# Kernel optimization log

Hardware: AMD Instinct MI355X
Metric: run time of the kernel (lower is better)

Reference implementation:

```python
import jax, jax.numpy as jnp
import numpy as np

B, T, D, H = 8, 1024, 768, 12
HD = D // H          # 64 head dim
WINDOW = 768         # sliding-window width hardcoded in the block
EPS = 1e-5

def _layer_norm(x, w, b):
    mu = jnp.mean(x, axis=-1, keepdims=True)
    var = jnp.mean(jnp.square(x - mu), axis=-1, keepdims=True)
    return (x - mu) * jax.lax.rsqrt(var + EPS) * w + b

def setup_inputs() -> dict:
    key = jax.random.key(0)
    ks = jax.random.split(key, 16)
    s = 0.02
    return {
        "x": jax.random.normal(ks[0], (B, T, D), jnp.float32),
        "attn_mask": jnp.ones((B, T), jnp.int32),
        "ln1_w": jnp.ones((D,), jnp.float32),
        "ln1_b": jnp.zeros((D,), jnp.float32),
        "w_attn": jax.random.normal(ks[1], (D, 3 * D), jnp.float32) * s,
        "b_attn": jnp.zeros((3 * D,), jnp.float32),
        "w_proj": jax.random.normal(ks[2], (D, D), jnp.float32) * s,
        "b_proj": jnp.zeros((D,), jnp.float32),
        "ln2_w": jnp.ones((D,), jnp.float32),
        "ln2_b": jnp.zeros((D,), jnp.float32),
        "w_fc": jax.random.normal(ks[3], (D, 4 * D), jnp.float32) * s,
        "b_fc": jnp.zeros((4 * D,), jnp.float32),
        "w_fc_proj": jax.random.normal(ks[4], (4 * D, D), jnp.float32) * s,
        "b_fc_proj": jnp.zeros((D,), jnp.float32),
    }

def reference(x, attn_mask, ln1_w, ln1_b, w_attn, b_attn, w_proj, b_proj,
              ln2_w, ln2_b, w_fc, b_fc, w_fc_proj, b_fc_proj):
    dtype = x.dtype
    # --- attention sub-block ---
    x1 = _layer_norm(x, ln1_w, ln1_b)
    qkv = x1 @ w_attn + b_attn                       # [B,T,3D]
    q, k, v = jnp.split(qkv, 3, axis=-1)
    q = q.reshape(B, T, H, HD).transpose(0, 2, 1, 3)  # [B,H,T,HD]
    k = k.reshape(B, T, H, HD).transpose(0, 2, 1, 3)
    v = v.reshape(B, T, H, HD).transpose(0, 2, 1, 3)
    # causal + sliding-window + padding mask (additive bias, as in source)
    i = jnp.arange(T)[:, None]
    j = jnp.arange(T)[None, :]
    keep = (j <= i) & (j >= i - WINDOW + 1)           # [T,T]
    keep = keep[None, None] & (attn_mask.astype(bool))[:, None, None, :]  # [B,1,T,T]
    mask_bias = jnp.where(keep, jnp.zeros((), dtype), jnp.full((), jnp.finfo(dtype).min, dtype))
    scale = 1.0 / np.sqrt(HD)
    scores = jnp.einsum('bhqd,bhkd->bhqk', q, k) * scale + mask_bias
    probs = jax.nn.softmax(scores, axis=-1)
    attn = jnp.einsum('bhqk,bhkd->bhqd', probs, v)    # [B,H,T,HD]
    attn = attn.transpose(0, 2, 1, 3).reshape(B, T, D)
    a = attn @ w_proj + b_proj
    x = x + a
    # --- MLP sub-block ---
    x3 = _layer_norm(x, ln2_w, ln2_b)
    h = jax.nn.gelu(x3 @ w_fc + b_fc, approximate=False)
    m = h @ w_fc_proj + b_fc_proj
    return x + m
```

## Files before the change

kernel.cpp:

```cpp
#include <hip/hip_runtime.h>
#include <hip/hip_bf16.h>
#include <math.h>

#define NB 8
#define NT 1024
#define ND 768
#define NH 12
#define HD 64
#define WINDOW 768
#define LN_EPS 1e-5f
#define NEGF -3.4028234663852886e38f
#define SCL2 0.18033688011112042f

static const int BT = NB * NT;

typedef __bf16 bf16x8 __attribute__((ext_vector_type(8)));
typedef float  f32x4  __attribute__((ext_vector_type(4)));
typedef unsigned short ushort_t;

__device__ __forceinline__ unsigned short f2bf(float f) {
    __hip_bfloat16 h = __float2bfloat16(f);
    return __builtin_bit_cast(unsigned short, h);
}

__device__ __forceinline__ void load_lds16(const void* g, void* l) {
    __builtin_amdgcn_global_load_lds((const __attribute__((address_space(1))) unsigned int*)g,
                                     (__attribute__((address_space(3))) unsigned int*)l,
                                     16, 0, 0);
}

__device__ __forceinline__ bf16x8 ds_read16(const ushort_t* p) {
    bf16x8 r;
    unsigned a = (unsigned)(size_t)(const __attribute__((address_space(3))) ushort_t*)p;
    asm volatile("ds_read_b128 %0, %1" : "=v"(r) : "v"(a));
    return r;
}

__global__ __launch_bounds__(256) void transpose_all(const float* __restrict__ w0, ushort_t* __restrict__ t0v,
                                                     const float* __restrict__ w1, ushort_t* __restrict__ t1v,
                                                     const float* __restrict__ w2, ushort_t* __restrict__ t2v,
                                                     const float* __restrict__ w3, ushort_t* __restrict__ t3v) {
    int bid = blockIdx.x;
    const float* w; ushort_t* wt; int K, N;
    if (bid < 1728)                    { w = w0; wt = t0v; K = 768;  N = 2304; }
    else if ((bid -= 1728) < 576)      { w = w1; wt = t1v; K = 768;  N = 768;  }
    else if ((bid -= 576) < 2304)      { w = w2; wt = t2v; K = 768;  N = 3072; }
    else       { bid -= 2304;            w = w3; wt = t3v; K = 3072; N = 768;  }
    const int nxt = N / 32;
    const int n0 = (bid % nxt) * 32, k0 = (bid / nxt) * 32;
    __shared__ float t[32][33];
    const int tx = threadIdx.x & 31, ty = threadIdx.x >> 5;
    for (int r = ty; r < 32; r += 8)
        t[r][tx] = w[(size_t)(k0 + r) * N + n0 + tx];
    __syncthreads();
    for (int r = ty; r < 32; r += 8)
        wt[(size_t)(n0 + r) * K + k0 + tx] = f2bf(t[tx][r]);
}

__global__ __launch_bounds__(256) void transpose_v(const ushort_t* __restrict__ qkvb,
                                                   ushort_t* __restrict__ vT) {
    const int t0 = blockIdx.x * 64;
    const int h = blockIdx.y, b = blockIdx.z;
    __shared__ ushort_t sm[64 * 72];
    const int tid = threadIdx.x;
    #pragma unroll
    for (int p = 0; p < 2; p++) {
        int idx = p * 256 + tid;
        int r = idx >> 3, c = idx & 7;
        *(bf16x8*)&sm[r * 72 + c * 8] =
            *(const bf16x8*)(qkvb + (size_t)(b * NT + t0 + r) * (3 * ND) + 2 * ND + h * HD + c * 8);
    }
    __syncthreads();
    #pragma unroll
    for (int p = 0; p < 2; p++) {
        int idx = p * 256 + tid;
        int d = idx >> 3, c2 = idx & 7;
        ushort_t tmp[8];
        #pragma unroll
        for (int j = 0; j < 8; j++) {
            int kp = c2 * 8 + j;
            int key = ((kp & 1) << 4) | ((kp >> 1) & 15) | (kp & 32);
            tmp[j] = sm[key * 72 + d];
        }
        *(bf16x8*)(vT + ((size_t)((b * NH + h) * HD + d)) * NT + t0 + c2 * 8) = *(bf16x8*)tmp;
    }
}

__global__ __launch_bounds__(256) void ln_kernel(const float* __restrict__ x,
                                                 const float* __restrict__ w,
                                                 const float* __restrict__ b,
                                                 ushort_t* __restrict__ out) {
    const int row  = blockIdx.x * 4 + (threadIdx.x >> 6);
    const int lane = threadIdx.x & 63;
    const float* xr = x + (size_t)row * ND;

    float4 v[3];
    #pragma unroll
    for (int s = 0; s < 3; s++) v[s] = *(const float4*)(xr + s * 256 + lane * 4);

    float sum = 0.f;
    #pragma unroll
    for (int s = 0; s < 3; s++) sum += v[s].x + v[s].y + v[s].z + v[s].w;
    #pragma unroll
    for (int off = 1; off < 64; off <<= 1) sum += __shfl_xor(sum, off, 64);
    const float mu = sum * (1.0f / ND);

    float var = 0.f;
    #pragma unroll
    for (int s = 0; s < 3; s++) {
        float a0 = v[s].x - mu, a1 = v[s].y - mu, a2 = v[s].z - mu, a3 = v[s].w - mu;
        var += a0 * a0 + a1 * a1 + a2 * a2 + a3 * a3;
    }
    #pragma unroll
    for (int off = 1; off < 64; off <<= 1) var += __shfl_xor(var, off, 64);
    const float rstd = rsqrtf(var * (1.0f / ND) + LN_EPS);

    #pragma unroll
    for (int s = 0; s < 3; s++) {
        const int col = s * 256 + lane * 4;
        float4 w4 = *(const float4*)(w + col);
        float4 b4 = *(const float4*)(b + col);
        ushort4 r;
        r.x = f2bf((v[s].x - mu) * rstd * w4.x + b4.x);
        r.y = f2bf((v[s].y - mu) * rstd * w4.y + b4.y);
        r.z = f2bf((v[s].z - mu) * rstd * w4.z + b4.z);
        r.w = f2bf((v[s].w - mu) * rstd * w4.w + b4.w);
        *(ushort4*)(out + (size_t)row * ND + col) = r;
    }
}

template <int EPI>
__global__ __launch_bounds__(256) void gemm_bt(const ushort_t* __restrict__ A,
                                               const ushort_t* __restrict__ Bt,
                                               const float* __restrict__ bias,
                                               const float* __restrict__ resid,
                                               void* __restrict__ Cout,
                                               int M, int N, int K) {
    __shared__ __align__(16) ushort_t smem[2][2][128 * 32];

    const int tid  = threadIdx.x;
    const int bm   = blockIdx.y * 128;
    const int bn   = blockIdx.x * 128;
    const int lane = tid & 63;
    const int wave = tid >> 6;
    const int wm   = (wave & 1) * 64;
    const int wn   = (wave >> 1) * 64;
    const int fcol = lane & 15;
    const int quad = lane >> 4;

    f32x4 acc[4][4] = {};

    const int srow = tid >> 2, scg = (tid & 3) * 8;

    auto issue = [&](int k0, int buf) {
        #pragma unroll
        for (int p = 0; p < 2; p++) {
            const int row = srow + p * 64;
            const int flat = (p * 256 + tid) * 8;
            load_lds16(A  + (size_t)(bm + row) * K + k0 + scg, &smem[buf][0][flat]);
            load_lds16(Bt + (size_t)(bn + row) * K + k0 + scg, &smem[buf][1][flat]);
        }
    };

    issue(0, 0);
    const int KT = K >> 5;
    for (int kt = 0; kt < KT; kt++) {
        const int cur = kt & 1;
        __syncthreads();
        if (kt + 1 < KT) issue((kt + 1) << 5, cur ^ 1);

        bf16x8 a[4], b[4];
        #pragma unroll
        for (int i = 0; i < 4; i++)
            a[i] = *(const bf16x8*)&smem[cur][0][(wm + i * 16 + fcol) * 32 + quad * 8];
        #pragma unroll
        for (int j = 0; j < 4; j++)
            b[j] = *(const bf16x8*)&smem[cur][1][(wn + j * 16 + fcol) * 32 + quad * 8];
        #pragma unroll
        for (int i = 0; i < 4; i++)
            #pragma unroll
            for (int j = 0; j < 4; j++)
                acc[i][j] = __builtin_amdgcn_mfma_f32_16x16x32_bf16(a[i], b[j], acc[i][j], 0, 0, 0);
    }

    if (EPI == 1) {
        #pragma unroll
        for (int j = 0; j < 4; j++) {
            const int gcol = bn + wn + j * 16 + fcol;
            const float bs = bias[gcol];
            #pragma unroll
            for (int i = 0; i < 4; i++) {
                #pragma unroll
                for (int r = 0; r < 4; r++) {
                    const int grow = bm + wm + i * 16 + quad * 4 + r;
                    float val = acc[i][j][r] + bs + resid[(size_t)grow * N + gcol];
                    ((float*)Cout)[(size_t)grow * N + gcol] = val;
                }
            }
        }
    } else {
        __syncthreads();
        ushort_t* Cs = &smem[0][0][0] + wave * (64 * 40);
        #pragma unroll
        for (int hh = 0; hh < 2; hh++) {
            #pragma unroll
            for (int jj = 0; jj < 2; jj++) {
                const int j = hh * 2 + jj;
                const float bs = bias[bn + wn + j * 16 + fcol];
                #pragma unroll
                for (int i = 0; i < 4; i++) {
                    #pragma unroll
                    for (int r = 0; r < 4; r++) {
                        float val = acc[i][j][r] + bs;
                        if (EPI == 2) {
                            float y = 0.7978845608028654f * (val + 0.044715f * val * val * val);
                            float t = 1.0f - 2.0f / (1.0f + __expf(2.0f * y));
                            val = 0.5f * val * (1.0f + t);
                        }
                        const int lr = i * 16 + quad * 4 + r;
                        Cs[lr * 40 + jj * 16 + fcol] = f2bf(val);
                    }
                }
            }
            #pragma unroll
            for (int p = 0; p < 4; p++) {
                const int cid = p * 64 + lane;
                const int lr = cid >> 2, ck = cid & 3;
                bf16x8 vv = *(const bf16x8*)&Cs[lr * 40 + ck * 8];
                *(bf16x8*)((ushort_t*)Cout + (size_t)(bm + wm + lr) * N + bn + wn + hh * 32 + ck * 8) = vv;
            }
        }
    }
}

template <int EPI, int NN, int KK>
__global__ __launch_bounds__(512, 2) void gemm256(const ushort_t* __restrict__ A,
                                                  const ushort_t* __restrict__ Bt,
                                                  const float* __restrict__ bias,
                                                  ushort_t* __restrict__ Cout) {
    extern __shared__ __align__(16) ushort_t lds[];

    const int tid  = threadIdx.x;
    const int lane = tid & 63;
    const int wave = tid >> 6;
    const int wr   = wave >> 2;
    const int wn   = wave & 3;
    const int fcol = lane & 15;
    const int quad = lane >> 4;

    const int nwg  = gridDim.x * gridDim.y;
    const int flat = blockIdx.y * gridDim.x + blockIdx.x;
    const int q8   = nwg >> 3;
    const int swz  = (flat & 7) * q8 + (flat >> 3);
    const int bm   = (swz / gridDim.x) * 256;
    const int bn   = (swz % gridDim.x) * 256;

    constexpr int KT  = KK >> 6;
    constexpr int NIT = KT >> 1;

    f32x4 acc[8][4] = {};
    bf16x8 ra[4][2];
    bf16x8 rb0[2][2], rb1[2][2];

    ushort_t* const Ab = lds;
    ushort_t* const Bb = lds + 32768;

    auto stA = [&](int kt, int h) {
        ushort_t* dst = Ab + ((((kt & 1) << 1) | h) << 13);
        const int kk = (kt < KT ? kt : 0) << 6;
        #pragma unroll
        for (int p = 0; p < 2; p++) {
            const int f = (p << 9) + tid;
            const int r = f >> 3, c = (f & 7) ^ (r & 7);
            const int gr = bm + ((r >> 6) << 7) + (h << 6) + (r & 63);
            load_lds16(A + (size_t)gr * KK + kk + c * 8, dst + f * 8);
        }
    };
    auto stB = [&](int kt, int h) {
        ushort_t* dst = Bb + ((((kt & 1) << 1) | h) << 13);
        const int kk = (kt < KT ? kt : 0) << 6;
        #pragma unroll
        for (int p = 0; p < 2; p++) {
            const int f = (p << 9) + tid;
            const int r = f >> 3, c = (f & 7) ^ (r & 7);
            const int gr = bn + ((r >> 5) << 6) + (h << 5) + (r & 31);
            load_lds16(Bt + (size_t)gr * KK + kk + c * 8, dst + f * 8);
        }
    };

#define SOFF(r, c) ((((r) << 3) + (((c) ^ ((r) & 7)))) << 3)
#define LOAD_A(PAR, MH) { const ushort_t* s_ = Ab + ((((PAR) << 1) | (MH)) << 13);   \
    _Pragma("unroll") for (int i2 = 0; i2 < 4; i2++)                                 \
    _Pragma("unroll") for (int ks = 0; ks < 2; ks++)                                 \
        ra[i2][ks] = ds_read16(&s_[SOFF(wr * 64 + i2 * 16 + fcol, ks * 4 + quad)]); }
#define LOAD_B(PAR, NH, RB) { const ushort_t* s_ = Bb + ((((PAR) << 1) | (NH)) << 13); \
    _Pragma("unroll") for (int j2 = 0; j2 < 2; j2++)                                 \
    _Pragma("unroll") for (int ks = 0; ks < 2; ks++)                                 \
        RB[j2][ks] = ds_read16(&s_[SOFF(wn * 32 + j2 * 16 + fcol, ks * 4 + quad)]); }
#define MMA(MH, NH, RB) {                                                            \
    __builtin_amdgcn_s_barrier();                                                    \
    asm volatile("s_waitcnt lgkmcnt(0)" ::: "memory");                               \
    __builtin_amdgcn_sched_barrier(0);                                               \
    __builtin_amdgcn_s_setprio(1);                                                   \
    _Pragma("unroll") for (int i2 = 0; i2 < 4; i2++)                                 \
    _Pragma("unroll") for (int j2 = 0; j2 < 2; j2++)                                 \
    _Pragma("unroll") for (int ks = 0; ks < 2; ks++)                                 \
        acc[(MH) * 4 + i2][(NH) * 2 + j2] = __builtin_amdgcn_mfma_f32_16x16x32_bf16( \
            ra[i2][ks], RB[j2][ks], acc[(MH) * 4 + i2][(NH) * 2 + j2], 0, 0, 0);     \
    __builtin_amdgcn_s_setprio(0);                                                   \
    __builtin_amdgcn_sched_barrier(0);                                               \
    __builtin_amdgcn_s_barrier(); }
#define VMW6() asm volatile("s_waitcnt vmcnt(6)" ::: "memory")

    stA(0, 0); stB(0, 0); stB(0, 1); stA(0, 1);
    stA(1, 0); stB(1, 0); stB(1, 1);
    VMW6();
    __builtin_amdgcn_s_barrier();

    #pragma unroll 1
    for (int it = 0; it < NIT; ++it) {
        const int E = it << 1, O = E + 1;
        LOAD_A(0, 0); LOAD_B(0, 0, rb0);
        stA(O, 1);
        MMA(0, 0, rb0);

        LOAD_B(0, 1, rb1);
        stA(E + 2, 0);
        MMA(0, 1, rb1);

        LOAD_A(0, 1);
        stB(E + 2, 0);
        MMA(1, 1, rb1);

        stB(E + 2, 1);
        VMW6();
        MMA(1, 0, rb0);

        LOAD_A(1, 0); LOAD_B(1, 0, rb0);
        stA(E + 2, 1);
        MMA(0, 0, rb0);

        LOAD_B(1, 1, rb1);
        stA(O + 2, 0);
        MMA(0, 1, rb1);

        LOAD_A(1, 1);
        stB(O + 2, 0);
        MMA(1, 1, rb1);

        stB(O + 2, 1);
        VMW6();
        MMA(1, 0, rb0);
    }

    asm volatile("s_waitcnt vmcnt(0)" ::: "memory");
    __builtin_amdgcn_s_barrier();

    ushort_t* Cs = lds + wave * (64 * 72);
    #pragma unroll
    for (int h = 0; h < 2; h++) {
        #pragma unroll
        for (int j = 0; j < 4; j++) {
            const float bs = bias[bn + wn * 64 + j * 16 + fcol];
            #pragma unroll
            for (int i2 = 0; i2 < 4; i2++) {
                #pragma unroll
                for (int r = 0; r < 4; r++) {
                    float val = acc[h * 4 + i2][j][r] + bs;
                    if (EPI == 2) {
                        float y = 0.7978845608028654f * (val + 0.044715f * val * val * val);
                        float t = 1.0f - 2.0f / (1.0f + __expf(2.0f * y));
                        val = 0.5f * val * (1.0f + t);
                    }
                    Cs[(i2 * 16 + quad * 4 + r) * 72 + j * 16 + fcol] = f2bf(val);
                }
            }
        }
        #pragma unroll
        for (int p = 0; p < 8; p++) {
            const int cid = (p << 6) + lane;
            const int lr = cid >> 3, ck = cid & 7;
            bf16x8 vv = *(const bf16x8*)&Cs[lr * 72 + ck * 8];
            *(bf16x8*)(Cout + (size_t)(bm + wr * 128 + h * 64 + lr) * NN + bn + wn * 64 + ck * 8) = vv;
        }
    }
#undef SOFF
#undef LOAD_A
#undef LOAD_B
#undef MMA
#undef VMW6
}

__global__ __launch_bounds__(256) void flash_attn_mfma(const ushort_t* __restrict__ qkvb,
                                                       const ushort_t* __restrict__ vT,
                                                       const int* __restrict__ amask,
                                                       ushort_t* __restrict__ out) {
    const int qt = 15 - blockIdx.x;
    const int h  = blockIdx.y;
    const int b  = blockIdx.z;
    const int q0 = qt * 64;

    __shared__ __align__(16) ushort_t QPs[64 * 64];
    __shared__ __align__(16) ushort_t Ks[2][64 * 64];
    __shared__ __align__(16) ushort_t Vts[2][64 * 64];

    const int tid  = threadIdx.x;
    const int lane = tid & 63;
    const int wave = tid >> 6;
    const int fcol = lane & 15;
    const int quad = lane >> 4;
    const int wq0  = wave * 16;

    #pragma unroll
    for (int p = 0; p < 2; p++) {
        int flat = p * 256 + tid;
        int r = flat >> 3, c = (flat & 7) ^ (r & 7);
        load_lds16(qkvb + (size_t)(b * NT + q0 + r) * (3 * ND) + h * HD + c * 8, &QPs[flat * 8]);
    }
    __syncthreads();

    bf16x8 aQ[2];
    {
        const int qr = wq0 + fcol;
        #pragma unroll
        for (int ks = 0; ks < 2; ks++) {
            int c = ks * 4 + quad;
            aQ[ks] = *(const bf16x8*)&QPs[qr * 64 + ((c ^ (qr & 7)) * 8)];
        }
    }

    bf16x8 bones;
    #pragma unroll
    for (int i = 0; i < 8; i++) bones[i] = (__bf16)1.0f;

    auto issueKV = [&](int cch, int buf) {
        const int kbase = cch * 64;
        #pragma unroll
        for (int p = 0; p < 2; p++) {
            int flat = p * 256 + tid;
            int r = flat >> 3, c = (flat & 7) ^ (r & 7);
            load_lds16(qkvb + (size_t)(b * NT + kbase + r) * (3 * ND) + ND + h * HD + c * 8,
                       &Ks[buf][flat * 8]);
            load_lds16(vT + ((size_t)((b * NH + h) * HD + r)) * NT + kbase + c * 8,
                       &Vts[buf][flat * 8]);
        }
    };

    f32x4 oacc[4] = {};
    f32x4 lacc = {};

    const int c_lo = (qt > 12) ? (qt - 12) : 0;
    issueKV(c_lo, 0);
    for (int cch = c_lo; cch <= qt; cch++) {
        const int cur = (cch - c_lo) & 1;
        const int kbase = cch * 64;
        __syncthreads();
        if (cch + 1 <= qt) issueKV(cch + 1, cur ^ 1);

        int am[4];
        #pragma unroll
        for (int jn = 0; jn < 4; jn++) am[jn] = amask[b * NT + kbase + jn * 16 + fcol];
        const int amok_lane = (am[0] != 0) & (am[1] != 0) & (am[2] != 0) & (am[3] != 0);
        const bool fast = (cch < qt) && (cch >= qt - 11) && __all(amok_lane);

        f32x4 sc[4] = {};
        #pragma unroll
        for (int ks = 0; ks < 2; ks++) {
            #pragma unroll
            for (int jn = 0; jn < 4; jn++) {
                const int kr = jn * 16 + fcol;
                bf16x8 bk = *(const bf16x8*)&Ks[cur][kr * 64 + (((ks * 4 + quad) ^ (kr & 7)) * 8)];
                sc[jn] = __builtin_amdgcn_mfma_f32_16x16x32_bf16(aQ[ks], bk, sc[jn], 0, 0, 0);
            }
        }

        float pvv[4][4];
        if (fast) {
            #pragma unroll
            for (int jn = 0; jn < 4; jn++)
                #pragma unroll
                for (int r = 0; r < 4; r++)
                    pvv[jn][r] = __builtin_amdgcn_exp2f(sc[jn][r] * SCL2);
        } else {
            #pragma unroll
            for (int jn = 0; jn < 4; jn++) {
                const int jg = kbase + jn * 16 + fcol;
                const bool amok = (am[jn] != 0);
                #pragma unroll
                for (int r = 0; r < 4; r++) {
                    const int ig = q0 + wq0 + quad * 4 + r;
                    bool keep = (jg <= ig) && (jg >= ig - (WINDOW - 1)) && amok;
                    float s = keep ? sc[jn][r] * SCL2 : -1e38f;
                    pvv[jn][r] = __builtin_amdgcn_exp2f(s);
                }
            }
        }

        #pragma unroll
        for (int half = 0; half < 2; half++) {
            const int cbase = half * 4 + (fcol >> 2);
            const int off = (fcol & 3) * 2;
            #pragma unroll
            for (int r = 0; r < 4; r++) {
                const int row = wq0 + quad * 4 + r;
                unsigned int pk = (unsigned int)f2bf(pvv[half * 2][r]) |
                                  ((unsigned int)f2bf(pvv[half * 2 + 1][r]) << 16);
                *(unsigned int*)&QPs[row * 64 + ((cbase ^ (row & 7)) * 8) + off] = pk;
            }
        }

        #pragma unroll
        for (int ks = 0; ks < 2; ks++) {
            const int pr = wq0 + fcol;
            bf16x8 ap = *(const bf16x8*)&QPs[pr * 64 + (((ks * 4 + quad) ^ (pr & 7)) * 8)];
            lacc = __builtin_amdgcn_mfma_f32_16x16x32_bf16(ap, bones, lacc, 0, 0, 0);
            #pragma unroll
            for (int jd = 0; jd < 4; jd++) {
                const int vr = jd * 16 + fcol;
                bf16x8 bv = *(const bf16x8*)&Vts[cur][vr * 64 + (((ks * 4 + quad) ^ (vr & 7)) * 8)];
                oacc[jd] = __builtin_amdgcn_mfma_f32_16x16x32_bf16(ap, bv, oacc[jd], 0, 0, 0);
            }
        }
    }

    #pragma unroll
    for (int r = 0; r < 4; r++) {
        const float inv = 1.0f / lacc[r];
        const size_t row = (size_t)(b * NT + q0 + wq0 + quad * 4 + r);
        #pragma unroll
        for (int jd = 0; jd < 4; jd++)
            out[row * ND + h * HD + jd * 16 + fcol] = f2bf(oacc[jd][r] * inv);
    }
}

extern "C" void kernel_launch(void* const* d_in, const int* in_sizes, int n_in,
                              void* d_out, int out_size, void* d_ws, size_t ws_size,
                              hipStream_t stream) {
    const float* x        = (const float*)d_in[0];
    const int*   amask    = (const int*)  d_in[1];
    const float* ln1_w    = (const float*)d_in[2];
    const float* ln1_b    = (const float*)d_in[3];
    const float* w_attn   = (const float*)d_in[4];
    const float* b_attn   = (const float*)d_in[5];
    const float* w_proj   = (const float*)d_in[6];
    const float* b_proj   = (const float*)d_in[7];
    const float* ln2_w    = (const float*)d_in[8];
    const float* ln2_b    = (const float*)d_in[9];
    const float* w_fc     = (const float*)d_in[10];
    const float* b_fc     = (const float*)d_in[11];
    const float* w_fcp    = (const float*)d_in[12];
    const float* b_fcp    = (const float*)d_in[13];
    float* out = (float*)d_out;

    ushort_t* ws = (ushort_t*)d_ws;
    ushort_t* qkvb   = ws;
    ushort_t* x1b    = qkvb + (size_t)BT * 3 * ND;
    ushort_t* attn_b = x1b + (size_t)BT * ND;
    ushort_t* hbuf   = attn_b + (size_t)BT * ND;
    ushort_t* vTb    = hbuf + (size_t)BT * 4 * ND;
    ushort_t* wA_T   = vTb + (size_t)BT * ND;
    ushort_t* wP_T   = wA_T + (size_t)2304 * 768;
    ushort_t* wF_T   = wP_T + (size_t)768 * 768;
    ushort_t* wFP_T  = wF_T + (size_t)3072 * 768;

    static bool attr_set = false;
    if (!attr_set) {
        hipFuncSetAttribute((const void*)gemm256<0, 2304, 768>, hipFuncAttributeMaxDynamicSharedMemorySize, 131072);
        hipFuncSetAttribute((const void*)gemm256<2, 3072, 768>, hipFuncAttributeMaxDynamicSharedMemorySize, 131072);
        attr_set = true;
    }

    transpose_all<<<6912, 256, 0, stream>>>(w_attn, wA_T, w_proj, wP_T, w_fc, wF_T, w_fcp, wFP_T);

    ln_kernel<<<BT / 4, 256, 0, stream>>>(x, ln1_w, ln1_b, x1b);
    gemm256<0, 2304, 768><<<dim3(2304 / 256, BT / 256), 512, 131072, stream>>>(x1b, wA_T, b_attn, qkvb);
    transpose_v<<<dim3(16, NH, NB), 256, 0, stream>>>(qkvb, vTb);
    flash_attn_mfma<<<dim3(16, NH, NB), 256, 0, stream>>>(qkvb, vTb, amask, attn_b);
    gemm_bt<1><<<dim3(768 / 128, BT / 128), 256, 0, stream>>>(attn_b, wP_T, b_proj, x, out, BT, ND, ND);
    ln_kernel<<<BT / 4, 256, 0, stream>>>(out, ln2_w, ln2_b, x1b);
    gemm256<2, 3072, 768><<<dim3(3072 / 256, BT / 256), 512, 131072, stream>>>(x1b, wF_T, b_fc, hbuf);
    gemm_bt<1><<<dim3(768 / 128, BT / 128), 256, 0, stream>>>(hbuf, wFP_T, b_fcp, out, out, BT, ND, 4 * ND);
}
```

Baseline: 382.3 us.

## Software-pipeline LDS fragment reads in GEMM with double-buffered registers and fewer barriers

```diff
diff --git a/kernel.cpp b/kernel.cpp
--- a/kernel.cpp
+++ b/kernel.cpp
@@ -248,19 +248,19 @@
     const int fcol = lane & 15;
     const int quad = lane >> 4;
 
-    const int nwg  = gridDim.x * gridDim.y;
-    const int flat = blockIdx.y * gridDim.x + blockIdx.x;
-    const int q8   = nwg >> 3;
-    const int swz  = (flat & 7) * q8 + (flat >> 3);
-    const int bm   = (swz / gridDim.x) * 256;
-    const int bn   = (swz % gridDim.x) * 256;
+    const int nwg   = gridDim.x * gridDim.y;
+    const int flatb = blockIdx.y * gridDim.x + blockIdx.x;
+    const int q8    = nwg >> 3;
+    const int swz   = (flatb & 7) * q8 + (flatb >> 3);
+    const int bm    = (swz / gridDim.x) * 256;
+    const int bn    = (swz % gridDim.x) * 256;
 
     constexpr int KT  = KK >> 6;
     constexpr int NIT = KT >> 1;
 
     f32x4 acc[8][4] = {};
-    bf16x8 ra[4][2];
-    bf16x8 rb0[2][2], rb1[2][2];
+    bf16x8 raA[4][2], raB[4][2];
+    bf16x8 rb[2][2][2];
 
     ushort_t* const Ab = lds;
     ushort_t* const Bb = lds + 32768;
@@ -289,72 +289,91 @@
     };
 
 #define SOFF(r, c) ((((r) << 3) + (((c) ^ ((r) & 7)))) << 3)
-#define LOAD_A(PAR, MH) { const ushort_t* s_ = Ab + ((((PAR) << 1) | (MH)) << 13);   \
-    _Pragma("unroll") for (int i2 = 0; i2 < 4; i2++)                                 \
-    _Pragma("unroll") for (int ks = 0; ks < 2; ks++)                                 \
-        ra[i2][ks] = ds_read16(&s_[SOFF(wr * 64 + i2 * 16 + fcol, ks * 4 + quad)]); }
-#define LOAD_B(PAR, NH, RB) { const ushort_t* s_ = Bb + ((((PAR) << 1) | (NH)) << 13); \
-    _Pragma("unroll") for (int j2 = 0; j2 < 2; j2++)                                 \
-    _Pragma("unroll") for (int ks = 0; ks < 2; ks++)                                 \
-        RB[j2][ks] = ds_read16(&s_[SOFF(wn * 32 + j2 * 16 + fcol, ks * 4 + quad)]); }
-#define MMA(MH, NH, RB) {                                                            \
-    __builtin_amdgcn_s_barrier();                                                    \
-    asm volatile("s_waitcnt lgkmcnt(0)" ::: "memory");                               \
-    __builtin_amdgcn_sched_barrier(0);                                               \
-    __builtin_amdgcn_s_setprio(1);                                                   \
-    _Pragma("unroll") for (int i2 = 0; i2 < 4; i2++)                                 \
-    _Pragma("unroll") for (int j2 = 0; j2 < 2; j2++)                                 \
-    _Pragma("unroll") for (int ks = 0; ks < 2; ks++)                                 \
-        acc[(MH) * 4 + i2][(NH) * 2 + j2] = __builtin_amdgcn_mfma_f32_16x16x32_bf16( \
-            ra[i2][ks], RB[j2][ks], acc[(MH) * 4 + i2][(NH) * 2 + j2], 0, 0, 0);     \
-    __builtin_amdgcn_s_setprio(0);                                                   \
-    __builtin_amdgcn_sched_barrier(0);                                               \
-    __builtin_amdgcn_s_barrier(); }
+#define RD_A(PAR, MH, RA) { const ushort_t* s_ = Ab + ((((PAR) << 1) | (MH)) << 13);  \
+    _Pragma("unroll") for (int i2 = 0; i2 < 4; i2++)                                  \
+    _Pragma("unroll") for (int ks = 0; ks < 2; ks++)                                  \
+        RA[i2][ks] = ds_read16(&s_[SOFF(wr * 64 + i2 * 16 + fcol, ks * 4 + quad)]); }
+#define RD_B(PAR, NH, BUF) { const ushort_t* s_ = Bb + ((((PAR) << 1) | (NH)) << 13); \
+    _Pragma("unroll") for (int j2 = 0; j2 < 2; j2++)                                  \
+    _Pragma("unroll") for (int ks = 0; ks < 2; ks++)                                  \
+        rb[BUF][j2][ks] = ds_read16(&s_[SOFF(wn * 32 + j2 * 16 + fcol, ks * 4 + quad)]); }
+#define LGKM(N) { asm volatile("s_waitcnt lgkmcnt(" #N ")" ::: "memory");             \
+    __builtin_amdgcn_sched_barrier(0); }
+#define MMA_CORE(MH, NH, BUF) {                                                       \
+    __builtin_amdgcn_sched_barrier(0);                                                \
+    __builtin_amdgcn_s_setprio(1);                                                    \
+    _Pragma("unroll") for (int i2 = 0; i2 < 4; i2++)                                  \
+    _Pragma("unroll") for (int j2 = 0; j2 < 2; j2++)                                  \
+    _Pragma("unroll") for (int ks = 0; ks < 2; ks++)                                  \
+        acc[(MH) * 4 + i2][(NH) * 2 + j2] = __builtin_amdgcn_mfma_f32_16x16x32_bf16(  \
+            (MH) ? raB[i2][ks] : raA[i2][ks], rb[BUF][j2][ks],                        \
+            acc[(MH) * 4 + i2][(NH) * 2 + j2], 0, 0, 0);                              \
+    __builtin_amdgcn_s_setprio(0);                                                    \
+    __builtin_amdgcn_sched_barrier(0); }
 #define VMW6() asm volatile("s_waitcnt vmcnt(6)" ::: "memory")
+#define BARR() asm volatile("s_barrier" ::: "memory")
 
     stA(0, 0); stB(0, 0); stB(0, 1); stA(0, 1);
     stA(1, 0); stB(1, 0); stB(1, 1);
     VMW6();
-    __builtin_amdgcn_s_barrier();
+    BARR();
+    RD_A(0, 0, raA);
+    RD_B(0, 0, 0);
 
     #pragma unroll 1
     for (int it = 0; it < NIT; ++it) {
         const int E = it << 1, O = E + 1;
-        LOAD_A(0, 0); LOAD_B(0, 0, rb0);
+        RD_B(0, 1, 1);
         stA(O, 1);
-        MMA(0, 0, rb0);
-
-        LOAD_B(0, 1, rb1);
+        LGKM(4);
+        MMA_CORE(0, 0, 0);
+        BARR();
+
+        RD_A(0, 1, raB);
         stA(E + 2, 0);
-        MMA(0, 1, rb1);
-
-        LOAD_A(0, 1);
+        LGKM(8);
+        MMA_CORE(0, 1, 1);
+        BARR();
+
         stB(E + 2, 0);
-        MMA(1, 1, rb1);
-
+        LGKM(0);
+        MMA_CORE(1, 1, 1);
+        BARR();
+
+        MMA_CORE(1, 0, 0);
         stB(E + 2, 1);
         VMW6();
-        MMA(1, 0, rb0);
-
-        LOAD_A(1, 0); LOAD_B(1, 0, rb0);
+        RD_A(1, 0, raA);
+        RD_B(1, 0, 1);
+        BARR();
+
+        RD_B(1, 1, 0);
         stA(E + 2, 1);
-        MMA(0, 0, rb0);
-
-        LOAD_B(1, 1, rb1);
+        LGKM(4);
+        MMA_CORE(0, 0, 1);
+        BARR();
+
+        RD_A(1, 1, raB);
         stA(O + 2, 0);
-        MMA(0, 1, rb1);
-
-        LOAD_A(1, 1);
+        LGKM(8);
+        MMA_CORE(0, 1, 0);
+        BARR();
+
         stB(O + 2, 0);
-        MMA(1, 1, rb1);
-
+        LGKM(0);
+        MMA_CORE(1, 1, 0);
+        BARR();
+
+        MMA_CORE(1, 0, 1);
         stB(O + 2, 1);
         VMW6();
-        MMA(1, 0, rb0);
-    }
-
-    asm volatile("s_waitcnt vmcnt(0)" ::: "memory");
-    __builtin_amdgcn_s_barrier();
+        RD_A(0, 0, raA);
+        RD_B(0, 0, 0);
+        BARR();
+    }
+
+    asm volatile("s_waitcnt vmcnt(0) lgkmcnt(0)" ::: "memory");
+    BARR();
 
     ushort_t* Cs = lds + wave * (64 * 72);
     #pragma unroll
@@ -385,10 +404,12 @@
         }
     }
 #undef SOFF
-#undef LOAD_A
-#undef LOAD_B
-#undef MMA
+#undef RD_A
+#undef RD_B
+#undef LGKM
+#undef MMA_CORE
 #undef VMW6
+#undef BARR
 }
 
 __global__ __launch_bounds__(256) void flash_attn_mfma(const ushort_t* __restrict__ qkvb,
```

Result: slower. 460.1 us (+20.3%).
